# Kernel tuning notes

Hardware: AMD Instinct MI355X
Metric: run time of the kernel (lower is better)

Reference implementation:

```python
import jax, jax.numpy as jnp
import numpy as np

# torch.optim.Adam defaults
LR = 1e-3
B1 = 0.9
B2 = 0.999
EPS = 1e-8


def setup_inputs() -> dict:
    key = jax.random.key(0)
    k1, k2 = jax.random.split(key)
    B, N_train, d = 128, 16384, 1024
    h = jax.random.normal(k1, (B, d), dtype=jnp.float32)
    H_train = jax.random.normal(k2, (N_train, d), dtype=jnp.float32)
    return {"h": h, "H_train": H_train, "n_epoch": 1000}


def reference(h, H_train, n_epoch):
    # preweights: [B, N_train], optimized by Adam for n_epoch steps
    B, N_train = h.shape[0], H_train.shape[0]

    def loss_fn(p):
        w = jax.nn.softmax(p, axis=-1)          # [B, N_train]
        H_approx = w @ H_train                   # [B, d]
        return jnp.sum((H_approx - h) ** 2)

    grad_fn = jax.grad(loss_fn)

    def step(carry, t):
        p, m, v = carry
        g = grad_fn(p)
        m = B1 * m + (1.0 - B1) * g
        v = B2 * v + (1.0 - B2) * (g * g)
        m_hat = m / (1.0 - B1 ** t)
        v_hat = v / (1.0 - B2 ** t)
        p = p - LR * m_hat / (jnp.sqrt(v_hat) + EPS)
        return (p, m, v), None

    z = jnp.zeros((B, N_train), dtype=jnp.float32)
    ts = jnp.arange(1, n_epoch + 1, dtype=jnp.float32)
    (p, _, _), _ = jax.lax.scan(step, (z, z, z), ts)
    return jax.nn.softmax(p, axis=-1)
```

## Files before the change

### kernel.cpp

```cpp
#include <hip/hip_runtime.h>
#include <math.h>

#define BB 128
#define NTR 16384
#define DD 1024
#define PN (BB*NTR)
#define CN (BB*DD)
#define HN (NTR*DD)
#define FWD_SLABS 32
#define BWD_SLABS 2

typedef short bf16x8 __attribute__((ext_vector_type(8)));
typedef float f32x2  __attribute__((ext_vector_type(2)));
typedef float f32x4v __attribute__((ext_vector_type(4)));

__device__ __forceinline__ ushort f2bf(float f) {
  uint u = __float_as_uint(f);
  return (ushort)((u + 0x7FFFu + ((u >> 16) & 1u)) >> 16);
}
__device__ __forceinline__ float bf2f(ushort h) { return __uint_as_float(((uint)h) << 16); }
__device__ __forceinline__ void split3(float f, ushort& a, ushort& b, ushort& c) {
  a = f2bf(f); float r1 = f - bf2f(a);
  b = f2bf(r1); float r2 = r1 - bf2f(b);
  c = f2bf(r2);
}
__device__ __forceinline__ void split2(float f, ushort& a, ushort& b) {
  a = f2bf(f); float r1 = f - bf2f(a);
  b = f2bf(r1);
}

__global__ __launch_bounds__(256) void k_prep(const float* __restrict__ H,
    ushort* __restrict__ H0, ushort* __restrict__ H1, ushort* __restrict__ H2)
{
  const size_t i = ((size_t)blockIdx.x * 256 + threadIdx.x) * 4;
  const float4 x = *(const float4*)(H + i);
  ushort a[4], b[4], c[4];
  split3(x.x, a[0], b[0], c[0]); split3(x.y, a[1], b[1], c[1]);
  split3(x.z, a[2], b[2], c[2]); split3(x.w, a[3], b[3], c[3]);
  *(ushort4*)(H0 + i) = make_ushort4(a[0], a[1], a[2], a[3]);
  *(ushort4*)(H1 + i) = make_ushort4(b[0], b[1], b[2], b[3]);
  *(ushort4*)(H2 + i) = make_ushort4(c[0], c[1], c[2], c[3]);
}

__global__ __launch_bounds__(256) void k_softmax_f(const float* __restrict__ p,
                                                   float* __restrict__ w) {
  const int row = blockIdx.x, tid = threadIdx.x;
  const float* pr = p + (size_t)row * NTR;
  float x[64]; float mx = -INFINITY;
#pragma unroll
  for (int i = 0; i < 64; ++i) { x[i] = pr[i*256 + tid]; mx = fmaxf(mx, x[i]); }
  __shared__ float red[256];
  red[tid] = mx; __syncthreads();
  for (int s = 128; s > 0; s >>= 1) { if (tid < s) red[tid] = fmaxf(red[tid], red[tid+s]); __syncthreads(); }
  mx = red[0]; __syncthreads();
  float sum = 0.f;
#pragma unroll
  for (int i = 0; i < 64; ++i) { x[i] = expf(x[i] - mx); sum += x[i]; }
  red[tid] = sum; __syncthreads();
  for (int s = 128; s > 0; s >>= 1) { if (tid < s) red[tid] += red[tid+s]; __syncthreads(); }
  const float inv = 1.0f / red[0];
  float* wr = w + (size_t)row * NTR;
#pragma unroll
  for (int i = 0; i < 64; ++i) wr[i*256 + tid] = x[i] * inv;
}

__global__ __launch_bounds__(256) void k_fwd_v(const float* __restrict__ w,
    const float* __restrict__ H, float* __restrict__ Cp)
{
  const int nt = blockIdx.x, tid = threadIdx.x;
  const int kbase = blockIdx.y * 512;
  Cp += (size_t)blockIdx.y * CN;
  __shared__ float As[8][128];
  __shared__ float Bs[8][64];
  const int tm = tid >> 4, tn = tid & 15;
  const int m0 = tm * 8, n0 = tn * 4;
  f32x2 acc[8][2];
#pragma unroll
  for (int i = 0; i < 8; ++i) { acc[i][0] = (f32x2){0.f,0.f}; acc[i][1] = (f32x2){0.f,0.f}; }
  for (int kk = 0; kk < 512; kk += 8) {
    {
      const int mm = tid >> 1, q = tid & 1;
      const float4 a4 = *(const float4*)(w + (size_t)mm*NTR + kbase + kk + q*4);
      As[q*4+0][mm]=a4.x; As[q*4+1][mm]=a4.y; As[q*4+2][mm]=a4.z; As[q*4+3][mm]=a4.w;
    }
    if (tid < 128) {
      const int r = tid >> 4, c = (tid & 15) * 4;
      *(float4*)&Bs[r][c] = *(const float4*)(H + (size_t)(kbase+kk+r)*DD + nt*64 + c);
    }
    __syncthreads();
#pragma unroll
    for (int k = 0; k < 8; ++k) {
      float a[8];
      *(float4*)&a[0] = *(const float4*)&As[k][m0];
      *(float4*)&a[4] = *(const float4*)&As[k][m0+4];
      const f32x2 b0 = *(const f32x2*)&Bs[k][n0];
      const f32x2 b1 = *(const f32x2*)&Bs[k][n0+2];
#pragma unroll
      for (int i = 0; i < 8; ++i) {
        const f32x2 ai = (f32x2){a[i], a[i]};
        acc[i][0] = __builtin_elementwise_fma(ai, b0, acc[i][0]);
        acc[i][1] = __builtin_elementwise_fma(ai, b1, acc[i][1]);
      }
    }
    __syncthreads();
  }
#pragma unroll
  for (int i = 0; i < 8; ++i)
    *(float4*)(Cp + (size_t)(m0+i)*DD + nt*64 + n0) =
        make_float4(acc[i][0].x, acc[i][0].y, acc[i][1].x, acc[i][1].y);
}

__global__ __launch_bounds__(256) void k_reduce_S2s(const float* __restrict__ X,
    const float* __restrict__ h,
    ushort* __restrict__ s0, ushort* __restrict__ s1)
{
  const size_t off = ((size_t)blockIdx.x * 256 + threadIdx.x) * 4;
  float4 s = make_float4(0.f, 0.f, 0.f, 0.f);
#pragma unroll 4
  for (int k = 0; k < FWD_SLABS; ++k) {
    const float4 c = *(const float4*)(X + (size_t)k * CN + off);
    s.x += c.x; s.y += c.y; s.z += c.z; s.w += c.w;
  }
  const float4 hh = *(const float4*)(h + off);
  float vals[4] = {2.f*(s.x-hh.x), 2.f*(s.y-hh.y), 2.f*(s.z-hh.z), 2.f*(s.w-hh.w)};
  ushort a[4], b[4];
#pragma unroll
  for (int e = 0; e < 4; ++e) split2(vals[e], a[e], b[e]);
  *(ushort4*)(s0 + off) = make_ushort4(a[0], a[1], a[2], a[3]);
  *(ushort4*)(s1 + off) = make_ushort4(b[0], b[1], b[2], b[3]);
}

__global__ __launch_bounds__(256, 2) void k_gemm3_bwd(
    const ushort* __restrict__ A0, const ushort* __restrict__ A1,
    const ushort* __restrict__ B0, const ushort* __restrict__ B1,
    float* __restrict__ C)
{
  __shared__ ushort lds[16384];
  const int tid = threadIdx.x;
  const int lane = tid & 63, wid = tid >> 6;
  const int wm = (wid >> 1) * 64, wn = (wid & 1) * 64;
  const int n0 = blockIdx.x * 128;
  const int kbase = blockIdx.y * 512;
  C += (size_t)blockIdx.y * PN;

  const ushort* Ap[2] = {A0, A1};
  const ushort* Bp[2] = {B0, B1};

  f32x4v acc[4][4];
#pragma unroll
  for (int i = 0; i < 4; ++i)
#pragma unroll
    for (int j = 0; j < 4; ++j) acc[i][j] = (f32x4v){0.f, 0.f, 0.f, 0.f};

  for (int kt = 0; kt < 16; ++kt) {
    const int kpos = kbase + (kt << 5);
#pragma unroll
    for (int c = 0; c < 4; ++c) {
      const int L = c*256 + tid;
      const int s = L >> 9, rr = L & 511;
      const int row = rr >> 2, slot = rr & 3;
      const int sl = slot ^ ((row >> 1) & 3);
      const ushort* src = Ap[s] + (size_t)row * DD + kpos + (sl << 3);
      __builtin_amdgcn_global_load_lds((const __attribute__((address_space(1))) void*)src,
          (__attribute__((address_space(3))) void*)&lds[(size_t)(c*256 + (wid << 6)) * 8], 16, 0, 0);
    }
#pragma unroll
    for (int c = 0; c < 4; ++c) {
      const int L = c*256 + tid;
      const int s = L >> 9, rr = L & 511;
      const int row = rr >> 2, slot = rr & 3;
      const int sl = slot ^ ((row >> 1) & 3);
      const ushort* src = Bp[s] + (size_t)(n0 + row) * DD + kpos + (sl << 3);
      __builtin_amdgcn_global_load_lds((const __attribute__((address_space(1))) void*)src,
          (__attribute__((address_space(3))) void*)&lds[8192 + (size_t)(c*256 + (wid << 6)) * 8], 16, 0, 0);
    }
    __syncthreads();

    bf16x8 bf[2][4];
#pragma unroll
    for (int s = 0; s < 2; ++s)
#pragma unroll
      for (int j = 0; j < 4; ++j) {
        const int n = wn + j*16 + (lane & 15);
        const int sl = (lane >> 4) ^ ((n >> 1) & 3);
        bf[s][j] = *(const bf16x8*)&lds[8192 + s*4096 + n*32 + sl*8];
      }
#pragma unroll
    for (int sa = 0; sa < 2; ++sa) {
      bf16x8 af[4];
#pragma unroll
      for (int i = 0; i < 4; ++i) {
        const int mrow = wm + i*16 + (lane & 15);
        const int sl = (lane >> 4) ^ ((mrow >> 1) & 3);
        af[i] = *(const bf16x8*)&lds[sa*4096 + mrow*32 + sl*8];
      }
#pragma unroll
      for (int sb = 0; sb < 2 - sa; ++sb)
#pragma unroll
        for (int i = 0; i < 4; ++i)
#pragma unroll
          for (int j = 0; j < 4; ++j)
            acc[i][j] = __builtin_amdgcn_mfma_f32_16x16x32_bf16(af[i], bf[sb][j], acc[i][j], 0, 0, 0);
    }
    __syncthreads();
  }
#pragma unroll
  for (int i = 0; i < 4; ++i) {
    const int rbase = wm + i*16 + ((lane >> 4) << 2);
#pragma unroll
    for (int j = 0; j < 4; ++j) {
      const int cg = n0 + wn + j*16 + (lane & 15);
#pragma unroll
      for (int r = 0; r < 4; ++r)
        C[(size_t)(rbase + r) * NTR + cg] = acc[i][j][r];
    }
  }
}

__global__ __launch_bounds__(256) void k_rdot_f(const float* __restrict__ X,
    const float* __restrict__ w, float* __restrict__ r)
{
  const int row = blockIdx.x, tid = threadIdx.x;
  const size_t rb = (size_t)row * NTR;
  float sum = 0.f;
  for (int c = 0; c < 16; ++c) {
    const size_t off = rb + (size_t)c * 1024 + tid * 4;
    float4 u  = *(const float4*)(X + off);
    const float4 u1 = *(const float4*)(X + (size_t)PN + off);
    u.x += u1.x; u.y += u1.y; u.z += u1.z; u.w += u1.w;
    const float4 ww = *(const float4*)(w + off);
    sum += ww.x*u.x + ww.y*u.y + ww.z*u.z + ww.w*u.w;
  }
  __shared__ float red[256];
  red[tid] = sum; __syncthreads();
  for (int s = 128; s > 0; s >>= 1) { if (tid < s) red[tid] += red[tid+s]; __syncthreads(); }
  if (tid == 0) r[row] = red[0];
}

__global__ __launch_bounds__(256) void k_adam_f(float* __restrict__ p,
    float* __restrict__ m, float* __restrict__ v,
    const float* __restrict__ w, const float* __restrict__ X,
    const float* __restrict__ r, float bc1, float bc2)
{
  const int bid = blockIdx.x;
  const float rr = r[bid >> 3];
  const size_t base = (size_t)bid * 2048 + threadIdx.x * 4;
#pragma unroll
  for (int part = 0; part < 2; ++part) {
    const size_t off = base + part * 1024;
    float4 u  = *(const float4*)(X + off);
    const float4 u1 = *(const float4*)(X + (size_t)PN + off);
    u.x += u1.x; u.y += u1.y; u.z += u1.z; u.w += u1.w;
    const float4 w4 = *(const float4*)(w + off);
    const float wv[4] = {w4.x, w4.y, w4.z, w4.w};
    const float uu[4] = {u.x, u.y, u.z, u.w};
    float4 p4 = *(float4*)(p + off);
    float4 m4 = *(float4*)(m + off);
    float4 v4 = *(float4*)(v + off);
    float* pp = (float*)&p4; float* mm = (float*)&m4; float* vv = (float*)&v4;
#pragma unroll
    for (int e = 0; e < 4; ++e) {
      const float g  = wv[e] * (uu[e] - rr);
      const float mn = 0.9f*mm[e] + 0.1f*g;
      const float vn = 0.999f*vv[e] + 0.001f*(g*g);
      const float mh = mn / bc1, vh = vn / bc2;
      pp[e] = pp[e] - 1e-3f * mh / (sqrtf(vh) + 1e-8f);
      mm[e] = mn; vv[e] = vn;
    }
    *(float4*)(p + off) = p4;
    *(float4*)(m + off) = m4;
    *(float4*)(v + off) = v4;
  }
}

extern "C" void kernel_launch(void* const* d_in, const int* in_sizes, int n_in,
                              void* d_out, int out_size, void* d_ws, size_t ws_size,
                              hipStream_t stream) {
  const float* h = (const float*)d_in[0];
  const float* H = (const float*)d_in[1];
  (void)in_sizes; (void)n_in; (void)out_size; (void)ws_size;
  const int n_epoch = 1000;

  float* p  = (float*)d_ws;
  float* m  = p + PN;
  float* v  = m + PN;
  float* w  = v + PN;
  float* X  = w + PN;
  float* r  = X + (size_t)2*PN;
  ushort* s0 = (ushort*)(r + 256);
  ushort* s1 = s0 + CN, *s2 = s1 + CN;
  ushort* H0 = s2 + CN, *H1 = H0 + HN, *H2 = H1 + HN;
  (void)s2;

  hipMemsetAsync(p, 0, (size_t)3*PN*sizeof(float), stream);
  k_prep<<<HN/1024, 256, 0, stream>>>(H, H0, H1, H2);

  for (int s = 1; s <= n_epoch; ++s) {
    k_softmax_f<<<BB, 256, 0, stream>>>(p, w);
    k_fwd_v<<<dim3(16, FWD_SLABS), 256, 0, stream>>>(w, H, X);
    k_reduce_S2s<<<CN/1024, 256, 0, stream>>>(X, h, s0, s1);
    k_gemm3_bwd<<<dim3(128, BWD_SLABS), 256, 0, stream>>>(s0, s1, H0, H1, X);
    k_rdot_f<<<BB, 256, 0, stream>>>(X, w, r);
    const float bc1 = 1.0f - powf(0.9f,   (float)s);
    const float bc2 = 1.0f - powf(0.999f, (float)s);
    k_adam_f<<<1024, 256, 0, stream>>>(p, m, v, w, X, r, bc1, bc2);
  }
  k_softmax_f<<<BB, 256, 0, stream>>>(p, (float*)d_out);
}
```

Baseline: 132.3 ms.

## Fuse row-dot reduction into backward GEMM epilogue and retile forward GEMM

The k_rdot_f kernel is removed. Each backward GEMM block now computes partial w·X row dots in its epilogue, writes them to a partials buffer, and k_adam_f reduces those partials in shared memory. The forward fp32 GEMM widens its N tile to 128 and halves the K slab so that 64 slabs are launched. The unused third bf16 split of H is also dropped from prep. Together these remove one launch and one full pass over X and w each epoch, at the cost of extra epilogue work and a larger slab reduction in k_reduce_S2s.

```diff
diff --git a/kernel.cpp b/kernel.cpp
--- a/kernel.cpp
+++ b/kernel.cpp
@@ -7,7 +7,7 @@
 #define PN (BB*NTR)
 #define CN (BB*DD)
 #define HN (NTR*DD)
-#define FWD_SLABS 32
+#define FWD_SLABS 64
 #define BWD_SLABS 2
 
 typedef short bf16x8 __attribute__((ext_vector_type(8)));
@@ -19,27 +19,21 @@
   return (ushort)((u + 0x7FFFu + ((u >> 16) & 1u)) >> 16);
 }
 __device__ __forceinline__ float bf2f(ushort h) { return __uint_as_float(((uint)h) << 16); }
-__device__ __forceinline__ void split3(float f, ushort& a, ushort& b, ushort& c) {
-  a = f2bf(f); float r1 = f - bf2f(a);
-  b = f2bf(r1); float r2 = r1 - bf2f(b);
-  c = f2bf(r2);
-}
 __device__ __forceinline__ void split2(float f, ushort& a, ushort& b) {
   a = f2bf(f); float r1 = f - bf2f(a);
   b = f2bf(r1);
 }
 
 __global__ __launch_bounds__(256) void k_prep(const float* __restrict__ H,
-    ushort* __restrict__ H0, ushort* __restrict__ H1, ushort* __restrict__ H2)
+    ushort* __restrict__ H0, ushort* __restrict__ H1)
 {
   const size_t i = ((size_t)blockIdx.x * 256 + threadIdx.x) * 4;
   const float4 x = *(const float4*)(H + i);
-  ushort a[4], b[4], c[4];
-  split3(x.x, a[0], b[0], c[0]); split3(x.y, a[1], b[1], c[1]);
-  split3(x.z, a[2], b[2], c[2]); split3(x.w, a[3], b[3], c[3]);
+  ushort a[4], b[4];
+  split2(x.x, a[0], b[0]); split2(x.y, a[1], b[1]);
+  split2(x.z, a[2], b[2]); split2(x.w, a[3], b[3]);
   *(ushort4*)(H0 + i) = make_ushort4(a[0], a[1], a[2], a[3]);
   *(ushort4*)(H1 + i) = make_ushort4(b[0], b[1], b[2], b[3]);
-  *(ushort4*)(H2 + i) = make_ushort4(c[0], c[1], c[2], c[3]);
 }
 
 __global__ __launch_bounds__(256) void k_softmax_f(const float* __restrict__ p,
@@ -68,24 +62,26 @@
     const float* __restrict__ H, float* __restrict__ Cp)
 {
   const int nt = blockIdx.x, tid = threadIdx.x;
-  const int kbase = blockIdx.y * 512;
+  const int kbase = blockIdx.y * 256;
   Cp += (size_t)blockIdx.y * CN;
   __shared__ float As[8][128];
-  __shared__ float Bs[8][64];
+  __shared__ float Bs[8][128];
   const int tm = tid >> 4, tn = tid & 15;
-  const int m0 = tm * 8, n0 = tn * 4;
-  f32x2 acc[8][2];
-#pragma unroll
-  for (int i = 0; i < 8; ++i) { acc[i][0] = (f32x2){0.f,0.f}; acc[i][1] = (f32x2){0.f,0.f}; }
-  for (int kk = 0; kk < 512; kk += 8) {
+  const int m0 = tm * 8, n0 = tn * 8;
+  f32x2 acc[8][4];
+#pragma unroll
+  for (int i = 0; i < 8; ++i)
+#pragma unroll
+    for (int j = 0; j < 4; ++j) acc[i][j] = (f32x2){0.f, 0.f};
+  for (int kk = 0; kk < 256; kk += 8) {
     {
       const int mm = tid >> 1, q = tid & 1;
       const float4 a4 = *(const float4*)(w + (size_t)mm*NTR + kbase + kk + q*4);
       As[q*4+0][mm]=a4.x; As[q*4+1][mm]=a4.y; As[q*4+2][mm]=a4.z; As[q*4+3][mm]=a4.w;
     }
-    if (tid < 128) {
-      const int r = tid >> 4, c = (tid & 15) * 4;
-      *(float4*)&Bs[r][c] = *(const float4*)(H + (size_t)(kbase+kk+r)*DD + nt*64 + c);
+    {
+      const int r = tid >> 5, c = (tid & 31) * 4;
+      *(float4*)&Bs[r][c] = *(const float4*)(H + (size_t)(kbase+kk+r)*DD + nt*128 + c);
     }
     __syncthreads();
 #pragma unroll
@@ -93,21 +89,27 @@
       float a[8];
       *(float4*)&a[0] = *(const float4*)&As[k][m0];
       *(float4*)&a[4] = *(const float4*)&As[k][m0+4];
-      const f32x2 b0 = *(const f32x2*)&Bs[k][n0];
-      const f32x2 b1 = *(const f32x2*)&Bs[k][n0+2];
+      f32x2 b[4];
+      b[0] = *(const f32x2*)&Bs[k][n0];
+      b[1] = *(const f32x2*)&Bs[k][n0+2];
+      b[2] = *(const f32x2*)&Bs[k][n0+4];
+      b[3] = *(const f32x2*)&Bs[k][n0+6];
 #pragma unroll
       for (int i = 0; i < 8; ++i) {
         const f32x2 ai = (f32x2){a[i], a[i]};
-        acc[i][0] = __builtin_elementwise_fma(ai, b0, acc[i][0]);
-        acc[i][1] = __builtin_elementwise_fma(ai, b1, acc[i][1]);
+#pragma unroll
+        for (int j = 0; j < 4; ++j)
+          acc[i][j] = __builtin_elementwise_fma(ai, b[j], acc[i][j]);
       }
     }
     __syncthreads();
   }
 #pragma unroll
-  for (int i = 0; i < 8; ++i)
-    *(float4*)(Cp + (size_t)(m0+i)*DD + nt*64 + n0) =
-        make_float4(acc[i][0].x, acc[i][0].y, acc[i][1].x, acc[i][1].y);
+  for (int i = 0; i < 8; ++i) {
+    float* dst = Cp + (size_t)(m0+i)*DD + nt*128 + n0;
+    *(float4*)dst     = make_float4(acc[i][0].x, acc[i][0].y, acc[i][1].x, acc[i][1].y);
+    *(float4*)(dst+4) = make_float4(acc[i][2].x, acc[i][2].y, acc[i][3].x, acc[i][3].y);
+  }
 }
 
 __global__ __launch_bounds__(256) void k_reduce_S2s(const float* __restrict__ X,
@@ -133,15 +135,18 @@
 __global__ __launch_bounds__(256, 2) void k_gemm3_bwd(
     const ushort* __restrict__ A0, const ushort* __restrict__ A1,
     const ushort* __restrict__ B0, const ushort* __restrict__ B1,
-    float* __restrict__ C)
+    const float* __restrict__ w,
+    float* __restrict__ C, float* __restrict__ rpart)
 {
   __shared__ ushort lds[16384];
+  __shared__ float rbuf[128][33];
   const int tid = threadIdx.x;
   const int lane = tid & 63, wid = tid >> 6;
   const int wm = (wid >> 1) * 64, wn = (wid & 1) * 64;
-  const int n0 = blockIdx.x * 128;
-  const int kbase = blockIdx.y * 512;
-  C += (size_t)blockIdx.y * PN;
+  const int bn = blockIdx.x, ks = blockIdx.y;
+  const int n0 = bn * 128;
+  const int kbase = ks * 512;
+  C += (size_t)ks * PN;
 
   const ushort* Ap[2] = {A0, A1};
   const ushort* Bp[2] = {B0, B1};
@@ -208,43 +213,40 @@
   for (int i = 0; i < 4; ++i) {
     const int rbase = wm + i*16 + ((lane >> 4) << 2);
 #pragma unroll
-    for (int j = 0; j < 4; ++j) {
-      const int cg = n0 + wn + j*16 + (lane & 15);
-#pragma unroll
-      for (int r = 0; r < 4; ++r)
-        C[(size_t)(rbase + r) * NTR + cg] = acc[i][j][r];
-    }
-  }
-}
-
-__global__ __launch_bounds__(256) void k_rdot_f(const float* __restrict__ X,
-    const float* __restrict__ w, float* __restrict__ r)
-{
-  const int row = blockIdx.x, tid = threadIdx.x;
-  const size_t rb = (size_t)row * NTR;
-  float sum = 0.f;
-  for (int c = 0; c < 16; ++c) {
-    const size_t off = rb + (size_t)c * 1024 + tid * 4;
-    float4 u  = *(const float4*)(X + off);
-    const float4 u1 = *(const float4*)(X + (size_t)PN + off);
-    u.x += u1.x; u.y += u1.y; u.z += u1.z; u.w += u1.w;
-    const float4 ww = *(const float4*)(w + off);
-    sum += ww.x*u.x + ww.y*u.y + ww.z*u.z + ww.w*u.w;
-  }
-  __shared__ float red[256];
-  red[tid] = sum; __syncthreads();
-  for (int s = 128; s > 0; s >>= 1) { if (tid < s) red[tid] += red[tid+s]; __syncthreads(); }
-  if (tid == 0) r[row] = red[0];
+    for (int r = 0; r < 4; ++r) {
+      const int row = rbase + r;
+      float s = 0.f;
+#pragma unroll
+      for (int j = 0; j < 4; ++j) {
+        const int cg = n0 + wn + j*16 + (lane & 15);
+        C[(size_t)row * NTR + cg] = acc[i][j][r];
+        s = fmaf(w[(size_t)row * NTR + cg], acc[i][j][r], s);
+      }
+      rbuf[row][((wid & 1) << 4) + (lane & 15)] = s;
+    }
+  }
+  __syncthreads();
+  if (tid < 128) {
+    float s = 0.f;
+#pragma unroll
+    for (int t = 0; t < 32; ++t) s += rbuf[tid][t];
+    rpart[((size_t)ks*128 + bn)*128 + tid] = s;
+  }
 }
 
 __global__ __launch_bounds__(256) void k_adam_f(float* __restrict__ p,
     float* __restrict__ m, float* __restrict__ v,
     const float* __restrict__ w, const float* __restrict__ X,
-    const float* __restrict__ r, float bc1, float bc2)
-{
-  const int bid = blockIdx.x;
-  const float rr = r[bid >> 3];
-  const size_t base = (size_t)bid * 2048 + threadIdx.x * 4;
+    const float* __restrict__ rpart, float bc1, float bc2)
+{
+  const int bid = blockIdx.x, tid = threadIdx.x;
+  const int row = bid >> 3;
+  __shared__ float red[256];
+  red[tid] = rpart[(size_t)tid*128 + row];
+  __syncthreads();
+  for (int s = 128; s > 0; s >>= 1) { if (tid < s) red[tid] += red[tid+s]; __syncthreads(); }
+  const float rr = red[0];
+  const size_t base = (size_t)bid * 2048 + tid * 4;
 #pragma unroll
   for (int part = 0; part < 2; ++part) {
     const size_t off = base + part * 1024;
@@ -286,24 +288,22 @@
   float* v  = m + PN;
   float* w  = v + PN;
   float* X  = w + PN;
-  float* r  = X + (size_t)2*PN;
-  ushort* s0 = (ushort*)(r + 256);
-  ushort* s1 = s0 + CN, *s2 = s1 + CN;
-  ushort* H0 = s2 + CN, *H1 = H0 + HN, *H2 = H1 + HN;
-  (void)s2;
+  float* rp = X + (size_t)4*PN;
+  ushort* s0 = (ushort*)(rp + 256*128);
+  ushort* s1 = s0 + CN;
+  ushort* H0 = s1 + CN, *H1 = H0 + HN;
 
   hipMemsetAsync(p, 0, (size_t)3*PN*sizeof(float), stream);
-  k_prep<<<HN/1024, 256, 0, stream>>>(H, H0, H1, H2);
+  k_prep<<<HN/1024, 256, 0, stream>>>(H, H0, H1);
 
   for (int s = 1; s <= n_epoch; ++s) {
     k_softmax_f<<<BB, 256, 0, stream>>>(p, w);
-    k_fwd_v<<<dim3(16, FWD_SLABS), 256, 0, stream>>>(w, H, X);
+    k_fwd_v<<<dim3(8, FWD_SLABS), 256, 0, stream>>>(w, H, X);
     k_reduce_S2s<<<CN/1024, 256, 0, stream>>>(X, h, s0, s1);
-    k_gemm3_bwd<<<dim3(128, BWD_SLABS), 256, 0, stream>>>(s0, s1, H0, H1, X);
-    k_rdot_f<<<BB, 256, 0, stream>>>(X, w, r);
+    k_gemm3_bwd<<<dim3(128, BWD_SLABS), 256, 0, stream>>>(s0, s1, H0, H1, w, X, rp);
     const float bc1 = 1.0f - powf(0.9f,   (float)s);
     const float bc2 = 1.0f - powf(0.999f, (float)s);
-    k_adam_f<<<1024, 256, 0, stream>>>(p, m, v, w, X, r, bc1, bc2);
+    k_adam_f<<<1024, 256, 0, stream>>>(p, m, v, w, X, rp, bc1, bc2);
   }
   k_softmax_f<<<BB, 256, 0, stream>>>(p, (float*)d_out);
 }
```

New measurement: 117.0 ms. 1.13x faster.
